# Optimization experiments

Hardware: AMD Instinct MI355X
Metric: run time of the kernel (lower is better)

The kernel has to match this reference:

```python
import jax, jax.numpy as jnp
import numpy as np

N_NODES = 50000
N_EDGES = 800000
D = 128


def _dense_params(key, d_in, d_out):
    kw, kb = jax.random.split(key)
    W = jax.random.normal(kw, (d_in, d_out), dtype=jnp.float32) / np.sqrt(d_in)
    b = jnp.zeros((d_out,), dtype=jnp.float32)
    return W, b


def setup_inputs() -> dict:
    key = jax.random.key(0)
    ks = jax.random.split(key, 9)
    nodes = jax.random.normal(ks[0], (N_NODES, D), dtype=jnp.float32)
    edges = jax.random.normal(ks[1], (N_EDGES, D), dtype=jnp.float32)
    senders = jax.random.randint(ks[2], (N_EDGES,), 0, N_NODES, dtype=jnp.int32)
    receivers = jax.random.randint(ks[3], (N_EDGES,), 0, N_NODES, dtype=jnp.int32)
    W_s1, b_s1 = _dense_params(ks[4], D, D)   # Dense on nodes -> sent_attributes_1
    W_r, b_r = _dense_params(ks[5], D, D)     # Dense on nodes -> received_attributes
    W_e, b_e = _dense_params(ks[6], D, D)     # Dense on edges
    W_att, b_att = _dense_params(ks[7], D, 1) # attention Dense -> scalar per edge
    W_m, b_m = _dense_params(ks[8], D, D)     # Dense on message (simple_update)
    return {
        "nodes": nodes, "edges": edges, "senders": senders, "receivers": receivers,
        "W_s1": W_s1, "b_s1": b_s1, "W_r": W_r, "b_r": b_r,
        "W_e": W_e, "b_e": b_e, "W_att": W_att, "b_att": b_att,
        "W_m": W_m, "b_m": b_m,
    }


def reference(nodes, edges, senders, receivers,
              W_s1, b_s1, W_r, b_r, W_e, b_e, W_att, b_att, W_m, b_m):
    n = nodes.shape[0]
    # dense projections on nodes, then gather along edges
    sent_1 = (nodes @ W_s1 + b_s1)[senders]          # [E, D]
    received = (nodes @ W_r + b_r)[receivers]        # [E, D]
    sent_2 = nodes[senders]                          # [E, D] (simple_update: raw gather)
    e_proj = edges @ W_e + b_e                       # [E, D]
    edges_new = sent_1 + e_proj + received           # add_features=True
    # attention: Dense(1) + leaky_relu, segment softmax over receivers
    att = jax.nn.leaky_relu(edges_new @ W_att + b_att)          # [E, 1]
    seg_max = jax.ops.segment_max(att, receivers, num_segments=n)
    expv = jnp.exp(att - seg_max[receivers])
    denom = jax.ops.segment_sum(expv, receivers, num_segments=n)
    weights = expv / denom[receivers]                            # [E, 1]
    # message: Dense on gathered sender features, weighted scatter-sum
    message = weights * (sent_2 @ W_m + b_m)                     # [E, D]
    nodes_new = jax.ops.segment_sum(message, receivers, num_segments=n)  # [N, D]
    return nodes_new, edges_new
```

## Files before the change

kernel.cpp:

```cpp
#include <hip/hip_runtime.h>
#include <hip/hip_bf16.h>
#include <cstdint>
#include <cstddef>

#define NN 50000
#define NE 800000
#define DD 128

typedef __attribute__((ext_vector_type(8))) short short8;
typedef __attribute__((ext_vector_type(4))) float f32x4;

__device__ __forceinline__ unsigned short f2bf(float f) {
  unsigned u = __float_as_uint(f);
  u = (u + 0x7FFFu + ((u >> 16) & 1u)) >> 16;
  return (unsigned short)u;
}

__global__ void k_prep(const float* __restrict__ Ws1, const float* __restrict__ Wr,
                       const float* __restrict__ Wm, const float* __restrict__ We,
                       unsigned short* __restrict__ Wt) {
  int i = blockIdx.x * blockDim.x + threadIdx.x;
  for (int idx = i; idx < 4 * DD * DD; idx += gridDim.x * blockDim.x) {
    int m = idx >> 14, r = idx & 16383, col = r >> 7, k = r & 127;
    const float* src = (m == 0) ? Ws1 : (m == 1) ? Wr : (m == 2) ? Wm : We;
    Wt[idx] = f2bf(src[k * DD + col]);
  }
}

__device__ __forceinline__ unsigned cvtpk(float lo, float hi) {
  unsigned r;
  asm("v_cvt_pk_bf16_f32 %0, %1, %2" : "=v"(r) : "v"(lo), "v"(hi));
  return r;
}

__device__ __forceinline__ short8 cvt8(f32x4 f0, f32x4 f1) {
  union { short8 s; unsigned u[4]; } t;
  t.u[0] = cvtpk(f0[0], f0[1]);
  t.u[1] = cvtpk(f0[2], f0[3]);
  t.u[2] = cvtpk(f1[0], f1[1]);
  t.u[3] = cvtpk(f1[2], f1[3]);
  return t.s;
}

__device__ __forceinline__ f32x4 unpk(uint2 u) {
  f32x4 v;
  v[0] = __uint_as_float(u.x << 16);
  v[1] = __uint_as_float(u.x & 0xFFFF0000u);
  v[2] = __uint_as_float(u.y << 16);
  v[3] = __uint_as_float(u.y & 0xFFFF0000u);
  return v;
}

__device__ __forceinline__ void stage_w(const unsigned short* __restrict__ Wt,
                                        char* __restrict__ lds, int tid) {
#pragma unroll
  for (int c = 0; c < 8; ++c) {
    int ci = tid * 8 + c;
    int col = ci >> 4, slot = ci & 15;
    uint4 v = *(const uint4*)(Wt + ci * 8);
    *(uint4*)(lds + col * 256 + ((slot ^ col) & 15) * 16) = v;
  }
}

__device__ __forceinline__ short8 read_w(const char* __restrict__ lds, int col, int slot) {
  return *(const short8*)(lds + col * 256 + ((slot ^ col) & 15) * 16);
}

__global__ __launch_bounds__(256, 4) void k_nodeproj(
    const float* __restrict__ nodes, const unsigned short* __restrict__ Wt,
    const float* __restrict__ b_s1, const float* __restrict__ b_r, const float* __restrict__ b_m,
    const float* __restrict__ b_e,
    unsigned* __restrict__ P1h, unsigned* __restrict__ Prh, unsigned* __restrict__ Pmh) {
  __shared__ char ldsW[32768];
  int m = blockIdx.y;
  int tid = threadIdx.x;
  stage_w(Wt + m * 16384, ldsW, tid);
  __syncthreads();
  const float* bias = (m == 0) ? b_s1 : (m == 1) ? b_r : b_m;
  unsigned* P = (m == 0) ? P1h : (m == 1) ? Prh : Pmh;
  int wid = tid >> 6, l = tid & 63;
  int lmod = l & 15, ldiv = l >> 4;
  int wave = blockIdx.x * 4 + wid, nw = gridDim.x * 4;
  for (int b = wave; b < NN / 16; b += nw) {
    int row = b * 16 + lmod;
    const float* nrow = nodes + (size_t)row * DD;
    short8 bb[4];
#pragma unroll
    for (int kk = 0; kk < 4; ++kk) {
      const f32x4* p = (const f32x4*)(nrow + kk * 32 + ldiv * 8);
      bb[kk] = cvt8(p[0], p[1]);
    }
    f32x4 acc[8] = {};
#pragma unroll
    for (int kk = 0; kk < 4; ++kk) {
#pragma unroll
      for (int rb = 0; rb < 8; ++rb) {
        short8 a = read_w(ldsW, rb * 16 + lmod, kk * 4 + ldiv);
        acc[rb] = __builtin_amdgcn_mfma_f32_16x16x32_bf16(a, bb[kk], acc[rb], 0, 0, 0);
      }
    }
#pragma unroll
    for (int rb = 0; rb < 8; ++rb) {
      int d0 = rb * 16 + ldiv * 4;
      f32x4 bv = *(const f32x4*)(bias + d0);
      if (m == 0) {
        f32x4 be = *(const f32x4*)(b_e + d0);
#pragma unroll
        for (int j = 0; j < 4; ++j) bv[j] += be[j];
      }
      f32x4 v = acc[rb];
#pragma unroll
      for (int j = 0; j < 4; ++j) v[j] += bv[j];
      uint2 pk;
      pk.x = cvtpk(v[0], v[1]);
      pk.y = cvtpk(v[2], v[3]);
      *(uint2*)(P + (size_t)row * (DD / 2) + d0 / 2) = pk;
    }
  }
}

__global__ __launch_bounds__(256, 5) void k_edge(
    const float* __restrict__ edges, const int* __restrict__ senders,
    const int* __restrict__ receivers, const unsigned short* __restrict__ WtE,
    const unsigned* __restrict__ P1h, const unsigned* __restrict__ Prh,
    const float* __restrict__ W_att, const float* __restrict__ b_att,
    float* __restrict__ out_edges, float* __restrict__ attb, int* __restrict__ cnt) {
  __shared__ char ldsW[32768];
  int tid = threadIdx.x;
  stage_w(WtE, ldsW, tid);
  __syncthreads();
  int wid = tid >> 6, l = tid & 63;
  int lmod = l & 15, ldiv = l >> 4;
  int wave = blockIdx.x * 4 + wid, nw = gridDim.x * 4;
  const int NB = NE / 16;
  float batt = b_att[0];

  for (int b = wave; b < NB; b += nw) {
    int e = b * 16 + lmod;
    const f32x4* erow = (const f32x4*)(edges + (size_t)e * DD);
    f32x4 cur[8];
#pragma unroll
    for (int q = 0; q < 8; ++q)
      cur[q] = __builtin_nontemporal_load(erow + ((q >> 1) * 8 + ldiv * 2 + (q & 1)));
    int s = senders[e], rc = receivers[e];

    short8 bb[4];
#pragma unroll
    for (int kk = 0; kk < 4; ++kk) bb[kk] = cvt8(cur[2 * kk], cur[2 * kk + 1]);

    f32x4 acc[8] = {};
#pragma unroll
    for (int kk = 0; kk < 4; ++kk) {
#pragma unroll
      for (int rb = 0; rb < 8; ++rb) {
        short8 a = read_w(ldsW, rb * 16 + lmod, kk * 4 + ldiv);
        acc[rb] = __builtin_amdgcn_mfma_f32_16x16x32_bf16(a, bb[kk], acc[rb], 0, 0, 0);
      }
    }

    const unsigned* p1 = P1h + (size_t)s * (DD / 2);
    const unsigned* pr = Prh + (size_t)rc * (DD / 2);
    float* oe = out_edges + (size_t)e * DD;
    float att = 0.f;
#pragma unroll
    for (int rb = 0; rb < 8; ++rb) {
      int d0 = rb * 16 + ldiv * 4;
      f32x4 g1 = unpk(*(const uint2*)(p1 + d0 / 2));
      f32x4 gr = unpk(*(const uint2*)(pr + d0 / 2));
      f32x4 wa = *(const f32x4*)(W_att + d0);
      f32x4 v = acc[rb];
#pragma unroll
      for (int j = 0; j < 4; ++j) {
        float x = v[j] + g1[j] + gr[j];
        v[j] = x;
        att += x * wa[j];
      }
      __builtin_nontemporal_store(v, (f32x4*)(oe + d0));
    }
    att += __shfl_xor(att, 16);
    att += __shfl_xor(att, 32);
    if (ldiv == 0) {
      float av = att + batt;
      av = (av >= 0.f) ? av : 0.01f * av;
      attb[e] = av;
      atomicAdd(&cnt[rc], 1);
    }
  }
}

__global__ __launch_bounds__(1024) void k_scan(const int* __restrict__ cnt,
                                               int* __restrict__ offs) {
  __shared__ int wsum[16];
  __shared__ int sbase;
  int t = threadIdx.x;
  int lane = t & 63, wid = t >> 6;
  if (t == 0) { sbase = 0; offs[0] = 0; }
  __syncthreads();
  for (int c = 0; c < 13; ++c) {
    int i0 = c * 4096 + t * 4;
    int v0 = 0, v1 = 0, v2 = 0, v3 = 0;
    if (i0 + 3 < NN) {
      int4 v = *(const int4*)(cnt + i0);
      v0 = v.x; v1 = v.y; v2 = v.z; v3 = v.w;
    } else {
      if (i0 + 0 < NN) v0 = cnt[i0 + 0];
      if (i0 + 1 < NN) v1 = cnt[i0 + 1];
      if (i0 + 2 < NN) v2 = cnt[i0 + 2];
      if (i0 + 3 < NN) v3 = cnt[i0 + 3];
    }
    int p1 = v0, p2 = p1 + v1, p3 = p2 + v2, p4 = p3 + v3;
    int x = p4;
#pragma unroll
    for (int d = 1; d < 64; d <<= 1) {
      int o = __shfl_up(x, d, 64);
      if (lane >= d) x += o;
    }
    if (lane == 63) wsum[wid] = x;
    int excl_lane = x - p4;
    __syncthreads();
    int wbase = 0, tot = 0;
#pragma unroll
    for (int w2 = 0; w2 < 16; ++w2) {
      int sv = wsum[w2];
      if (w2 < wid) wbase += sv;
      tot += sv;
    }
    int base = sbase + wbase + excl_lane;
    if (i0 + 0 < NN) offs[i0 + 1] = base + p1;
    if (i0 + 1 < NN) offs[i0 + 2] = base + p2;
    if (i0 + 2 < NN) offs[i0 + 3] = base + p3;
    if (i0 + 3 < NN) offs[i0 + 4] = base + p4;
    __syncthreads();
    if (t == 0) sbase += tot;
    __syncthreads();
  }
}

__global__ void k_fill(const int* __restrict__ receivers, const int* __restrict__ offs,
                       int* __restrict__ cursor, int* __restrict__ eidx) {
  int e = blockIdx.x * 256 + threadIdx.x;
  if (e < NE) {
    int rc = receivers[e];
    int pos = offs[rc] + atomicAdd(&cursor[rc], 1);
    eidx[pos] = e;
  }
}

__global__ __launch_bounds__(256) void k_node(
    const int* __restrict__ offs, const int* __restrict__ eidx,
    const int* __restrict__ senders, const float* __restrict__ attb,
    const unsigned* __restrict__ Pmh, float* __restrict__ out_nodes) {
  int wid = threadIdx.x >> 6, l = threadIdx.x & 63;
  int n = blockIdx.x * 4 + wid;
  if (n >= NN) return;
  int start = offs[n], end = offs[n + 1];
  float m = -3.4e38f, denom = 0.f, ax = 0.f, ay = 0.f;
  for (int c = start; c < end; c += 64) {
    int rem = end - c;
    if (rem > 64) rem = 64;
    float a_l = -3.4e38f;
    int s_l = 0;
    if (l < rem) {
      int e = eidx[c + l];
      a_l = attb[e];
      s_l = senders[e];
    }
    float cm = a_l;
#pragma unroll
    for (int d = 1; d < 64; d <<= 1) cm = fmaxf(cm, __shfl_xor(cm, d));
    if (cm > m) {
      float sc = __expf(m - cm);
      denom *= sc; ax *= sc; ay *= sc;
      m = cm;
    }
#pragma unroll 8
    for (int i = 0; i < rem; ++i) {
      float a = __shfl(a_l, i);
      int s = __shfl(s_l, i);
      float w = __expf(a - m);
      denom += w;
      unsigned u = Pmh[(size_t)s * (DD / 2) + l];
      float vx = __uint_as_float(u << 16);
      float vy = __uint_as_float(u & 0xFFFF0000u);
      ax += w * vx;
      ay += w * vy;
    }
  }
  float2 o = {0.f, 0.f};
  if (end > start) {
    float inv = 1.f / denom;
    o.x = ax * inv;
    o.y = ay * inv;
  }
  *(float2*)(out_nodes + (size_t)n * DD + l * 2) = o;
}

extern "C" void kernel_launch(void* const* d_in, const int* in_sizes, int n_in,
                              void* d_out, int out_size, void* d_ws, size_t ws_size,
                              hipStream_t stream) {
  (void)in_sizes; (void)n_in; (void)out_size; (void)ws_size;
  const float* nodes = (const float*)d_in[0];
  const float* edges = (const float*)d_in[1];
  const int* senders = (const int*)d_in[2];
  const int* receivers = (const int*)d_in[3];
  const float* W_s1 = (const float*)d_in[4];
  const float* b_s1 = (const float*)d_in[5];
  const float* W_r = (const float*)d_in[6];
  const float* b_r = (const float*)d_in[7];
  const float* W_e = (const float*)d_in[8];
  const float* b_e = (const float*)d_in[9];
  const float* W_att = (const float*)d_in[10];
  const float* b_att = (const float*)d_in[11];
  const float* W_m = (const float*)d_in[12];
  const float* b_m = (const float*)d_in[13];

  float* out_nodes = (float*)d_out;
  float* out_edges = out_nodes + (size_t)NN * DD;

  char* w = (char*)d_ws;
  unsigned short* Wt = (unsigned short*)w; w += (size_t)4 * DD * DD * 2;
  unsigned* P1h = (unsigned*)w; w += (size_t)NN * (DD / 2) * 4;
  unsigned* Prh = (unsigned*)w; w += (size_t)NN * (DD / 2) * 4;
  unsigned* Pmh = (unsigned*)w; w += (size_t)NN * (DD / 2) * 4;
  float* attb = (float*)w; w += (size_t)NE * 4;
  int* eidx = (int*)w; w += (size_t)NE * 4;
  int* cnt = (int*)w; w += (size_t)NN * 4;
  int* cursor = (int*)w; w += (size_t)NN * 4;
  int* offs = (int*)w; w += (size_t)(NN + 1) * 4;

  hipMemsetAsync(cnt, 0, (size_t)NN * 8, stream);

  k_prep<<<64, 256, 0, stream>>>(W_s1, W_r, W_m, W_e, Wt);
  k_nodeproj<<<dim3(256, 3), 256, 0, stream>>>(nodes, Wt, b_s1, b_r, b_m, b_e, P1h, Prh, Pmh);
  k_edge<<<1280, 256, 0, stream>>>(edges, senders, receivers, Wt + 3 * 16384,
                                   P1h, Prh, W_att, b_att, out_edges, attb, cnt);
  k_scan<<<1, 1024, 0, stream>>>(cnt, offs);
  k_fill<<<(NE + 255) / 256, 256, 0, stream>>>(receivers, offs, cursor, eidx);
  k_node<<<NN / 4, 256, 0, stream>>>(offs, eidx, senders, attb, Pmh, out_nodes);
}
```

Baseline: 452.2 us.

## Build receiver CSR first and process edges in receiver-sorted order

Moves the histogram/scan/fill stage ahead of the edge kernel and stores (edge, sender, receiver) tuples in receiver-sorted order. The edge kernel walks this sorted order, so receiver projection gathers are reused and attention scores are written contiguously for the node kernel, removing the eidx and senders indirection there. The cost is an extra histogram pass, a 16-byte tuple array, and edge rows and outputs now accessed in permuted order. The edge kernel also moves to 512-thread blocks.

```diff
diff --git a/kernel.cpp b/kernel.cpp
--- a/kernel.cpp
+++ b/kernel.cpp
@@ -51,11 +51,12 @@
   return v;
 }
 
+template <int NT>
 __device__ __forceinline__ void stage_w(const unsigned short* __restrict__ Wt,
                                         char* __restrict__ lds, int tid) {
 #pragma unroll
-  for (int c = 0; c < 8; ++c) {
-    int ci = tid * 8 + c;
+  for (int c = 0; c < 2048 / NT; ++c) {
+    int ci = tid * (2048 / NT) + c;
     int col = ci >> 4, slot = ci & 15;
     uint4 v = *(const uint4*)(Wt + ci * 8);
     *(uint4*)(lds + col * 256 + ((slot ^ col) & 15) * 16) = v;
@@ -74,7 +75,7 @@
   __shared__ char ldsW[32768];
   int m = blockIdx.y;
   int tid = threadIdx.x;
-  stage_w(Wt + m * 16384, ldsW, tid);
+  stage_w<256>(Wt + m * 16384, ldsW, tid);
   __syncthreads();
   const float* bias = (m == 0) ? b_s1 : (m == 1) ? b_r : b_m;
   unsigned* P = (m == 0) ? P1h : (m == 1) ? Prh : Pmh;
@@ -119,73 +120,9 @@
   }
 }
 
-__global__ __launch_bounds__(256, 5) void k_edge(
-    const float* __restrict__ edges, const int* __restrict__ senders,
-    const int* __restrict__ receivers, const unsigned short* __restrict__ WtE,
-    const unsigned* __restrict__ P1h, const unsigned* __restrict__ Prh,
-    const float* __restrict__ W_att, const float* __restrict__ b_att,
-    float* __restrict__ out_edges, float* __restrict__ attb, int* __restrict__ cnt) {
-  __shared__ char ldsW[32768];
-  int tid = threadIdx.x;
-  stage_w(WtE, ldsW, tid);
-  __syncthreads();
-  int wid = tid >> 6, l = tid & 63;
-  int lmod = l & 15, ldiv = l >> 4;
-  int wave = blockIdx.x * 4 + wid, nw = gridDim.x * 4;
-  const int NB = NE / 16;
-  float batt = b_att[0];
-
-  for (int b = wave; b < NB; b += nw) {
-    int e = b * 16 + lmod;
-    const f32x4* erow = (const f32x4*)(edges + (size_t)e * DD);
-    f32x4 cur[8];
-#pragma unroll
-    for (int q = 0; q < 8; ++q)
-      cur[q] = __builtin_nontemporal_load(erow + ((q >> 1) * 8 + ldiv * 2 + (q & 1)));
-    int s = senders[e], rc = receivers[e];
-
-    short8 bb[4];
-#pragma unroll
-    for (int kk = 0; kk < 4; ++kk) bb[kk] = cvt8(cur[2 * kk], cur[2 * kk + 1]);
-
-    f32x4 acc[8] = {};
-#pragma unroll
-    for (int kk = 0; kk < 4; ++kk) {
-#pragma unroll
-      for (int rb = 0; rb < 8; ++rb) {
-        short8 a = read_w(ldsW, rb * 16 + lmod, kk * 4 + ldiv);
-        acc[rb] = __builtin_amdgcn_mfma_f32_16x16x32_bf16(a, bb[kk], acc[rb], 0, 0, 0);
-      }
-    }
-
-    const unsigned* p1 = P1h + (size_t)s * (DD / 2);
-    const unsigned* pr = Prh + (size_t)rc * (DD / 2);
-    float* oe = out_edges + (size_t)e * DD;
-    float att = 0.f;
-#pragma unroll
-    for (int rb = 0; rb < 8; ++rb) {
-      int d0 = rb * 16 + ldiv * 4;
-      f32x4 g1 = unpk(*(const uint2*)(p1 + d0 / 2));
-      f32x4 gr = unpk(*(const uint2*)(pr + d0 / 2));
-      f32x4 wa = *(const f32x4*)(W_att + d0);
-      f32x4 v = acc[rb];
-#pragma unroll
-      for (int j = 0; j < 4; ++j) {
-        float x = v[j] + g1[j] + gr[j];
-        v[j] = x;
-        att += x * wa[j];
-      }
-      __builtin_nontemporal_store(v, (f32x4*)(oe + d0));
-    }
-    att += __shfl_xor(att, 16);
-    att += __shfl_xor(att, 32);
-    if (ldiv == 0) {
-      float av = att + batt;
-      av = (av >= 0.f) ? av : 0.01f * av;
-      attb[e] = av;
-      atomicAdd(&cnt[rc], 1);
-    }
-  }
+__global__ void k_hist(const int* __restrict__ receivers, int* __restrict__ cnt) {
+  int e = blockIdx.x * 256 + threadIdx.x;
+  if (e < NE) atomicAdd(&cnt[receivers[e]], 1);
 }
 
 __global__ __launch_bounds__(1024) void k_scan(const int* __restrict__ cnt,
@@ -236,20 +173,93 @@
   }
 }
 
-__global__ void k_fill(const int* __restrict__ receivers, const int* __restrict__ offs,
-                       int* __restrict__ cursor, int* __restrict__ eidx) {
+__global__ void k_fill(const int* __restrict__ senders, const int* __restrict__ receivers,
+                       const int* __restrict__ offs, int* __restrict__ cursor,
+                       uint4* __restrict__ esr) {
   int e = blockIdx.x * 256 + threadIdx.x;
   if (e < NE) {
     int rc = receivers[e];
     int pos = offs[rc] + atomicAdd(&cursor[rc], 1);
-    eidx[pos] = e;
+    uint4 v;
+    v.x = (unsigned)e; v.y = (unsigned)senders[e]; v.z = (unsigned)rc; v.w = 0u;
+    esr[pos] = v;
+  }
+}
+
+__global__ __launch_bounds__(512, 8) void k_edge(
+    const float* __restrict__ edges, const uint4* __restrict__ esr,
+    const unsigned short* __restrict__ WtE,
+    const unsigned* __restrict__ P1h, const unsigned* __restrict__ Prh,
+    const float* __restrict__ W_att, const float* __restrict__ b_att,
+    float* __restrict__ out_edges, float* __restrict__ attc) {
+  __shared__ char ldsW[32768];
+  int tid = threadIdx.x;
+  stage_w<512>(WtE, ldsW, tid);
+  __syncthreads();
+  int wid = tid >> 6, l = tid & 63;
+  int lmod = l & 15, ldiv = l >> 4;
+  int wave = blockIdx.x * 8 + wid, nw = gridDim.x * 8;
+  const int NB = NE / 16;
+  float batt = b_att[0];
+
+  for (int b = wave; b < NB; b += nw) {
+    int pos = b * 16 + lmod;
+    uint4 es = esr[pos];
+    int e = (int)es.x, s = (int)es.y, rc = (int)es.z;
+
+    const f32x4* erow = (const f32x4*)(edges + (size_t)e * DD);
+    f32x4 cur[8];
+#pragma unroll
+    for (int q = 0; q < 8; ++q)
+      cur[q] = __builtin_nontemporal_load(erow + ((q >> 1) * 8 + ldiv * 2 + (q & 1)));
+
+    short8 bb[4];
+#pragma unroll
+    for (int kk = 0; kk < 4; ++kk) bb[kk] = cvt8(cur[2 * kk], cur[2 * kk + 1]);
+
+    f32x4 acc[8] = {};
+#pragma unroll
+    for (int kk = 0; kk < 4; ++kk) {
+#pragma unroll
+      for (int rb = 0; rb < 8; ++rb) {
+        short8 a = read_w(ldsW, rb * 16 + lmod, kk * 4 + ldiv);
+        acc[rb] = __builtin_amdgcn_mfma_f32_16x16x32_bf16(a, bb[kk], acc[rb], 0, 0, 0);
+      }
+    }
+
+    const unsigned* p1 = P1h + (size_t)s * (DD / 2);
+    const unsigned* pr = Prh + (size_t)rc * (DD / 2);
+    float* oe = out_edges + (size_t)e * DD;
+    float att = 0.f;
+#pragma unroll
+    for (int rb = 0; rb < 8; ++rb) {
+      int d0 = rb * 16 + ldiv * 4;
+      f32x4 g1 = unpk(*(const uint2*)(p1 + d0 / 2));
+      f32x4 gr = unpk(*(const uint2*)(pr + d0 / 2));
+      f32x4 wa = *(const f32x4*)(W_att + d0);
+      f32x4 v = acc[rb];
+#pragma unroll
+      for (int j = 0; j < 4; ++j) {
+        float x = v[j] + g1[j] + gr[j];
+        v[j] = x;
+        att += x * wa[j];
+      }
+      __builtin_nontemporal_store(v, (f32x4*)(oe + d0));
+    }
+    att += __shfl_xor(att, 16);
+    att += __shfl_xor(att, 32);
+    if (ldiv == 0) {
+      float av = att + batt;
+      av = (av >= 0.f) ? av : 0.01f * av;
+      attc[pos] = av;
+    }
   }
 }
 
 __global__ __launch_bounds__(256) void k_node(
-    const int* __restrict__ offs, const int* __restrict__ eidx,
-    const int* __restrict__ senders, const float* __restrict__ attb,
-    const unsigned* __restrict__ Pmh, float* __restrict__ out_nodes) {
+    const int* __restrict__ offs, const uint4* __restrict__ esr,
+    const float* __restrict__ attc, const unsigned* __restrict__ Pmh,
+    float* __restrict__ out_nodes) {
   int wid = threadIdx.x >> 6, l = threadIdx.x & 63;
   int n = blockIdx.x * 4 + wid;
   if (n >= NN) return;
@@ -261,9 +271,8 @@
     float a_l = -3.4e38f;
     int s_l = 0;
     if (l < rem) {
-      int e = eidx[c + l];
-      a_l = attb[e];
-      s_l = senders[e];
+      a_l = attc[c + l];
+      s_l = (int)esr[c + l].y;
     }
     float cm = a_l;
 #pragma unroll
@@ -322,8 +331,8 @@
   unsigned* P1h = (unsigned*)w; w += (size_t)NN * (DD / 2) * 4;
   unsigned* Prh = (unsigned*)w; w += (size_t)NN * (DD / 2) * 4;
   unsigned* Pmh = (unsigned*)w; w += (size_t)NN * (DD / 2) * 4;
-  float* attb = (float*)w; w += (size_t)NE * 4;
-  int* eidx = (int*)w; w += (size_t)NE * 4;
+  float* attc = (float*)w; w += (size_t)NE * 4;
+  uint4* esr = (uint4*)w; w += (size_t)NE * 16;
   int* cnt = (int*)w; w += (size_t)NN * 4;
   int* cursor = (int*)w; w += (size_t)NN * 4;
   int* offs = (int*)w; w += (size_t)(NN + 1) * 4;
@@ -331,10 +340,11 @@
   hipMemsetAsync(cnt, 0, (size_t)NN * 8, stream);
 
   k_prep<<<64, 256, 0, stream>>>(W_s1, W_r, W_m, W_e, Wt);
+  k_hist<<<(NE + 255) / 256, 256, 0, stream>>>(receivers, cnt);
+  k_scan<<<1, 1024, 0, stream>>>(cnt, offs);
+  k_fill<<<(NE + 255) / 256, 256, 0, stream>>>(senders, receivers, offs, cursor, esr);
   k_nodeproj<<<dim3(256, 3), 256, 0, stream>>>(nodes, Wt, b_s1, b_r, b_m, b_e, P1h, Prh, Pmh);
-  k_edge<<<1280, 256, 0, stream>>>(edges, senders, receivers, Wt + 3 * 16384,
-                                   P1h, Prh, W_att, b_att, out_edges, attb, cnt);
-  k_scan<<<1, 1024, 0, stream>>>(cnt, offs);
-  k_fill<<<(NE + 255) / 256, 256, 0, stream>>>(receivers, offs, cursor, eidx);
-  k_node<<<NN / 4, 256, 0, stream>>>(offs, eidx, senders, attb, Pmh, out_nodes);
-}
+  k_edge<<<1024, 512, 0, stream>>>(edges, esr, Wt + 3 * 16384,
+                                   P1h, Prh, W_att, b_att, out_edges, attc);
+  k_node<<<NN / 4, 256, 0, stream>>>(offs, esr, attc, Pmh, out_nodes);
+}
```

Result: slower. 540.7 us (+19.6%).

## Software-pipeline edge tile loads with double buffering in k_edge

Applied to the files above, without the earlier changes.

The edge kernel now prefetches the next 16-edge tile (edge rows plus sender/receiver indices) into a second register buffer while the current tile runs its MFMA work. The P1/Pr gathers are issued before the matmul so their latency overlaps with compute. The attention weights are staged once in LDS. To pay for the extra registers, occupancy is lowered from 5 to 3 blocks per CU and the grid shrinks from 1280 to 768 blocks, which reduces the number of waves available to hide latency.

```diff
diff --git a/kernel.cpp b/kernel.cpp
--- a/kernel.cpp
+++ b/kernel.cpp
@@ -119,15 +119,17 @@
   }
 }
 
-__global__ __launch_bounds__(256, 5) void k_edge(
+__global__ __launch_bounds__(256, 3) void k_edge(
     const float* __restrict__ edges, const int* __restrict__ senders,
     const int* __restrict__ receivers, const unsigned short* __restrict__ WtE,
     const unsigned* __restrict__ P1h, const unsigned* __restrict__ Prh,
     const float* __restrict__ W_att, const float* __restrict__ b_att,
     float* __restrict__ out_edges, float* __restrict__ attb, int* __restrict__ cnt) {
   __shared__ char ldsW[32768];
+  __shared__ float attw[DD];
   int tid = threadIdx.x;
   stage_w(WtE, ldsW, tid);
+  if (tid < DD / 4) ((f32x4*)attw)[tid] = ((const f32x4*)W_att)[tid];
   __syncthreads();
   int wid = tid >> 6, l = tid & 63;
   int lmod = l & 15, ldiv = l >> 4;
@@ -135,19 +137,38 @@
   const int NB = NE / 16;
   float batt = b_att[0];
 
-  for (int b = wave; b < NB; b += nw) {
+  int b = wave;
+  if (b >= NB) return;
+
+  f32x4 A[8], B[8];
+  int sA, rcA, sB, rcB;
+
+  auto load_grp = [&](f32x4(&G)[8], int& S, int& R, int bt) {
+    int en = bt * 16 + lmod;
+    const f32x4* erow = (const f32x4*)(edges + (size_t)en * DD);
+#pragma unroll
+    for (int q = 0; q < 8; ++q)
+      G[q] = __builtin_nontemporal_load(erow + ((q >> 1) * 8 + ldiv * 2 + (q & 1)));
+    S = senders[en];
+    R = receivers[en];
+  };
+
+  auto body = [&](f32x4(&CUR)[8], int& SC, int& RC, f32x4(&NXT)[8], int& SN, int& RN) {
     int e = b * 16 + lmod;
-    const f32x4* erow = (const f32x4*)(edges + (size_t)e * DD);
-    f32x4 cur[8];
-#pragma unroll
-    for (int q = 0; q < 8; ++q)
-      cur[q] = __builtin_nontemporal_load(erow + ((q >> 1) * 8 + ldiv * 2 + (q & 1)));
-    int s = senders[e], rc = receivers[e];
-
+    const unsigned* p1 = P1h + (size_t)SC * (DD / 2);
+    const unsigned* pr = Prh + (size_t)RC * (DD / 2);
+    uint2 g1[8], gr[8];
+#pragma unroll
+    for (int rb = 0; rb < 8; ++rb) {
+      int d2 = rb * 8 + ldiv * 2;
+      g1[rb] = *(const uint2*)(p1 + d2);
+      gr[rb] = *(const uint2*)(pr + d2);
+    }
+    int bn = b + nw;
+    if (bn < NB) load_grp(NXT, SN, RN, bn);
     short8 bb[4];
 #pragma unroll
-    for (int kk = 0; kk < 4; ++kk) bb[kk] = cvt8(cur[2 * kk], cur[2 * kk + 1]);
-
+    for (int kk = 0; kk < 4; ++kk) bb[kk] = cvt8(CUR[2 * kk], CUR[2 * kk + 1]);
     f32x4 acc[8] = {};
 #pragma unroll
     for (int kk = 0; kk < 4; ++kk) {
@@ -157,21 +178,18 @@
         acc[rb] = __builtin_amdgcn_mfma_f32_16x16x32_bf16(a, bb[kk], acc[rb], 0, 0, 0);
       }
     }
-
-    const unsigned* p1 = P1h + (size_t)s * (DD / 2);
-    const unsigned* pr = Prh + (size_t)rc * (DD / 2);
     float* oe = out_edges + (size_t)e * DD;
     float att = 0.f;
 #pragma unroll
     for (int rb = 0; rb < 8; ++rb) {
       int d0 = rb * 16 + ldiv * 4;
-      f32x4 g1 = unpk(*(const uint2*)(p1 + d0 / 2));
-      f32x4 gr = unpk(*(const uint2*)(pr + d0 / 2));
-      f32x4 wa = *(const f32x4*)(W_att + d0);
+      f32x4 g1v = unpk(g1[rb]);
+      f32x4 grv = unpk(gr[rb]);
+      f32x4 wa = *(const f32x4*)(attw + d0);
       f32x4 v = acc[rb];
 #pragma unroll
       for (int j = 0; j < 4; ++j) {
-        float x = v[j] + g1[j] + gr[j];
+        float x = v[j] + g1v[j] + grv[j];
         v[j] = x;
         att += x * wa[j];
       }
@@ -183,8 +201,17 @@
       float av = att + batt;
       av = (av >= 0.f) ? av : 0.01f * av;
       attb[e] = av;
-      atomicAdd(&cnt[rc], 1);
-    }
+      atomicAdd(&cnt[RC], 1);
+    }
+    b = bn;
+  };
+
+  load_grp(A, sA, rcA, b);
+  while (true) {
+    body(A, sA, rcA, B, sB, rcB);
+    if (b >= NB) break;
+    body(B, sB, rcB, A, sA, rcA);
+    if (b >= NB) break;
   }
 }
 
@@ -332,8 +359,8 @@
 
   k_prep<<<64, 256, 0, stream>>>(W_s1, W_r, W_m, W_e, Wt);
   k_nodeproj<<<dim3(256, 3), 256, 0, stream>>>(nodes, Wt, b_s1, b_r, b_m, b_e, P1h, Prh, Pmh);
-  k_edge<<<1280, 256, 0, stream>>>(edges, senders, receivers, Wt + 3 * 16384,
-                                   P1h, Prh, W_att, b_att, out_edges, attb, cnt);
+  k_edge<<<768, 256, 0, stream>>>(edges, senders, receivers, Wt + 3 * 16384,
+                                  P1h, Prh, W_att, b_att, out_edges, attb, cnt);
   k_scan<<<1, 1024, 0, stream>>>(cnt, offs);
   k_fill<<<(NE + 255) / 256, 256, 0, stream>>>(receivers, offs, cursor, eidx);
   k_node<<<NN / 4, 256, 0, stream>>>(offs, eidx, senders, attb, Pmh, out_nodes);
```

After: 452.3 us. No clear change (+0.0%).
